# Kernel tuning notes

Measured on AMD Instinct MI355X. Metric: run time of the kernel, lower is better.

## Reference

```python
import jax, jax.numpy as jnp
import numpy as np

N, G, E, H, Z = 50000, 2000, 800000, 512, 64
BN_EPS = 1e-5


def setup_inputs() -> dict:
    key = jax.random.key(0)
    ks = jax.random.split(key, 10)
    x = jax.random.normal(ks[0], (N, G), dtype=jnp.float32)
    edge_index = jax.random.randint(ks[1], (2, E), 0, N, dtype=jnp.int32)
    s1 = 1.0 / np.sqrt(G)
    s2 = 1.0 / np.sqrt(H)
    return {
        "x": x,
        "edge_index": edge_index,
        "W1l": jax.random.normal(ks[2], (G, H), dtype=jnp.float32) * s1,
        "b1": jnp.zeros((H,), jnp.float32),
        "W1r": jax.random.normal(ks[3], (G, H), dtype=jnp.float32) * s1,
        "bn_gamma": jax.random.uniform(ks[4], (H,), dtype=jnp.float32) + 0.5,
        "bn_beta": jax.random.normal(ks[5], (H,), dtype=jnp.float32) * 0.1,
        "bn_mean": jax.random.normal(ks[6], (H,), dtype=jnp.float32) * 0.1,
        "bn_var": jax.random.uniform(ks[7], (H,), dtype=jnp.float32) + 0.5,
        "W2l": jax.random.normal(ks[8], (H, Z), dtype=jnp.float32) * s2,
        "b2": jnp.zeros((Z,), jnp.float32),
        "W2r": jax.random.normal(ks[9], (H, Z), dtype=jnp.float32) * s2,
    }


def _sage_conv(h, src, dst, Wl, bl, Wr, n_nodes):
    # mean aggregation of source features at destination nodes
    msg = h[src]  # [E, D] gather
    agg = jax.ops.segment_sum(msg, dst, num_segments=n_nodes)
    cnt = jax.ops.segment_sum(jnp.ones((src.shape[0],), h.dtype), dst, num_segments=n_nodes)
    agg = agg / jnp.maximum(cnt, 1.0)[:, None]
    # PyG SAGEConv: lin_l(agg) + lin_r(x), bias only on lin_l
    return agg @ Wl + bl + h @ Wr


def reference(x, edge_index, W1l, b1, W1r, bn_gamma, bn_beta, bn_mean, bn_var, W2l, b2, W2r):
    src, dst = edge_index[0], edge_index[1]
    n = x.shape[0]
    h = _sage_conv(x, src, dst, W1l, b1, W1r, n)  # [N, H]
    # BatchNorm1d (eval mode: running stats) + ReLU; dropout is identity at inference
    h = (h - bn_mean) * (bn_gamma / jnp.sqrt(bn_var + BN_EPS)) + bn_beta
    h = jax.nn.relu(h)
    z = _sage_conv(h, src, dst, W2l, b2, W2r, n)  # [N, Z]
    return z
```

## Files before the change

kernel.cpp:

```cpp
#include <hip/hip_runtime.h>


#define BN_EPS 1e-5f
#define GK 2000
#define KP 2048
#define NT1C 63
#define NT1P 64
#define NT2 16

typedef __attribute__((ext_vector_type(8))) short bf16x8;
typedef __attribute__((ext_vector_type(4))) float f32x4;
typedef unsigned short u16x8 __attribute__((ext_vector_type(8)));

__device__ inline unsigned short f2bf(float f) {
    union { float f; unsigned u; } v; v.f = f;
    unsigned r = (v.u + 0x7fffu + ((v.u >> 16) & 1u)) >> 16;
    return (unsigned short)r;
}
__device__ inline float bf2f(unsigned short u) {
    union { unsigned u; float f; } v; v.u = ((unsigned)u) << 16;
    return v.f;
}

#define GLL16(gp, lp) __builtin_amdgcn_global_load_lds( \
    (const __attribute__((address_space(1))) void*)(gp), \
    (__attribute__((address_space(3))) void*)(lp), 16, 0, 0)

__global__ void count_kernel(const int* __restrict__ ei, int E, int* __restrict__ cnt) {
    int i = blockIdx.x * blockDim.x + threadIdx.x;
    if (i < E) atomicAdd(&cnt[ei[E + i]], 1);
}

__global__ __launch_bounds__(1024) void scan_kernel(const int* __restrict__ cnt,
                                                    int* __restrict__ row_start, int n) {
    __shared__ int part[1024];
    int t = threadIdx.x;
    int chunk = (n + 1023) >> 10;
    int lo = t * chunk;
    int hi = lo + chunk; if (hi > n) hi = n;
    int s = 0;
    for (int i = lo; i < hi; ++i) s += cnt[i];
    part[t] = s;
    __syncthreads();
    for (int off = 1; off < 1024; off <<= 1) {
        int add = (t >= off) ? part[t - off] : 0;
        __syncthreads();
        part[t] += add;
        __syncthreads();
    }
    int run = (t == 0) ? 0 : part[t - 1];
    for (int i = lo; i < hi; ++i) { row_start[i] = run; run += cnt[i]; }
    if (t == 1023) row_start[n] = part[1023];
}

__global__ void fill_kernel(const int* __restrict__ ei, int E,
                            const int* __restrict__ row_start,
                            int* __restrict__ cnt, int* __restrict__ colidx) {
    int i = blockIdx.x * blockDim.x + threadIdx.x;
    if (i < E) {
        int d = ei[E + i];
        int p = atomicSub(&cnt[d], 1) - 1;
        colidx[row_start[d] + p] = ei[i];
    }
}

__global__ __launch_bounds__(256) void conv_kernel(const float* __restrict__ x,
                                                   unsigned short* __restrict__ xb) {
    int row = blockIdx.x;
    int k8 = threadIdx.x;
    unsigned short us[8];
    if (k8 < 250) {
        const float4* p = (const float4*)(x + (size_t)row * 2000 + k8 * 8);
        float4 v0 = p[0], v1 = p[1];
        us[0]=f2bf(v0.x); us[1]=f2bf(v0.y); us[2]=f2bf(v0.z); us[3]=f2bf(v0.w);
        us[4]=f2bf(v1.x); us[5]=f2bf(v1.y); us[6]=f2bf(v1.z); us[7]=f2bf(v1.w);
    } else {
#pragma unroll
        for (int j = 0; j < 8; ++j) us[j] = 0;
    }
    *(u16x8*)&xb[(size_t)row * 2048 + k8 * 8] = *(u16x8*)us;
}

__global__ __launch_bounds__(256) void prep_bt(const float* __restrict__ W1l,
                                               const float* __restrict__ W1r,
                                               unsigned short* __restrict__ BT) {
    int idx = blockIdx.x * 256 + threadIdx.x;
    int c  = idx >> 8;
    int k0 = (idx & 255) << 3;
    const float* W = (c < 512) ? (W1l + c) : (W1r + (c - 512));
    unsigned short us[8];
#pragma unroll
    for (int j = 0; j < 8; ++j) {
        int k = k0 + j;
        float v = (k < GK) ? W[(size_t)k * 512] : 0.0f;
        us[j] = f2bf(v);
    }
    *(u16x8*)&BT[(size_t)c * KP + k0] = *(u16x8*)us;
}

__global__ __launch_bounds__(256) void prep_bt2(const float* __restrict__ W2l,
                                                const float* __restrict__ W2r,
                                                unsigned short* __restrict__ BT2) {
    int idx = blockIdx.x * 256 + threadIdx.x;
    int c  = idx >> 6;
    int k0 = (idx & 63) << 3;
    const float* W = (c < 64) ? (W2l + c) : (W2r + (c - 64));
    unsigned short us[8];
#pragma unroll
    for (int j = 0; j < 8; ++j) us[j] = f2bf(W[(size_t)(k0 + j) * 64]);
    *(u16x8*)&BT2[(size_t)c * 512 + k0] = *(u16x8*)us;
}

__global__ __launch_bounds__(512) void gemm1_256(
    const unsigned short* __restrict__ xb, int M,
    const unsigned short* __restrict__ BT,
    unsigned short* __restrict__ Y)
{
    __shared__ __align__(16) unsigned short As[3][8192];
    __shared__ __align__(16) unsigned short Bs[3][8192];

    const int t = threadIdx.x, wid = t >> 6, lane = t & 63;
    const int nbr = (M + 255) >> 8;
    const int nwg = nbr * 4;
    const int b   = blockIdx.x;
    int swz;
    if ((nwg & 7) == 0) swz = (b & 7) * (nwg >> 3) + (b >> 3);
    else swz = b;
    const int row0 = (swz >> 2) << 8;
    const int col0 = (swz & 3) << 8;

    const int c0 = t, c1 = t + 512;
    const int g0 = ((c0 & 3) ^ ((c0 >> 3) & 3)) << 3;
    const int g1 = ((c1 & 3) ^ ((c1 >> 3) & 3)) << 3;
    int ra0 = row0 + (c0 >> 2); if (ra0 >= M) ra0 = M - 1;
    int ra1 = row0 + (c1 >> 2); if (ra1 >= M) ra1 = M - 1;
    const unsigned short* aS0 = xb + (size_t)ra0 * KP + g0;
    const unsigned short* aS1 = xb + (size_t)ra1 * KP + g1;
    const unsigned short* bS0 = BT + (size_t)(col0 + (c0 >> 2)) * KP + g0;
    const unsigned short* bS1 = BT + (size_t)(col0 + (c1 >> 2)) * KP + g1;

    const int wr = wid >> 2, wc = wid & 3;
    const int fr16 = lane & 15;
    const int gswr = ((lane >> 4) ^ ((fr16 >> 1) & 3)) << 4;

    f32x4 acc[8][4];
#pragma unroll
    for (int m = 0; m < 8; ++m)
#pragma unroll
        for (int n = 0; n < 4; ++n) acc[m][n] = (f32x4)0.0f;

#define STG(kt, buf) do {                                          \
        unsigned short* ab_ = &As[buf][0];                         \
        unsigned short* bb_ = &Bs[buf][0];                         \
        GLL16(aS0 + (size_t)(kt) * 32, ab_ + c0 * 8);              \
        GLL16(aS1 + (size_t)(kt) * 32, ab_ + c1 * 8);              \
        GLL16(bS0 + (size_t)(kt) * 32, bb_ + c0 * 8);              \
        GLL16(bS1 + (size_t)(kt) * 32, bb_ + c1 * 8);              \
    } while (0)

    STG(0, 0);
    STG(1, 1);

    int rb = 0;
    for (int it = 0; it < NT1P; ++it) {
        if (it == NT1P - 1) {
            asm volatile("s_waitcnt vmcnt(0)" ::: "memory");
        } else {
            asm volatile("s_waitcnt vmcnt(4)" ::: "memory");
        }
        __builtin_amdgcn_s_barrier();
        __builtin_amdgcn_sched_barrier(0);

        const char* Ab = (const char*)&As[rb][0];
        const char* Bb = (const char*)&Bs[rb][0];
        bf16x8 af[8], bfr[4];
#pragma unroll
        for (int m = 0; m < 8; ++m)
            af[m] = *(const bf16x8*)(Ab + ((wr * 128 + m * 16 + fr16) << 6) + gswr);
#pragma unroll
        for (int n = 0; n < 4; ++n)
            bfr[n] = *(const bf16x8*)(Bb + ((wc * 64 + n * 16 + fr16) << 6) + gswr);

        if (it + 2 < NT1P) {
            int wb = rb + 2; if (wb >= 3) wb -= 3;
            STG(it + 2, wb);
        }

        __builtin_amdgcn_s_setprio(1);
#pragma unroll
        for (int m = 0; m < 8; ++m)
#pragma unroll
            for (int n = 0; n < 4; ++n)
                acc[m][n] = __builtin_amdgcn_mfma_f32_16x16x32_bf16(
                    af[m], bfr[n], acc[m][n], 0, 0, 0);
        __builtin_amdgcn_s_setprio(0);

        rb = (rb == 2) ? 0 : rb + 1;
    }
#undef STG

    const int crow = (lane >> 4) << 2;
#pragma unroll
    for (int m = 0; m < 8; ++m) {
        int rbase = row0 + wr * 128 + m * 16 + crow;
#pragma unroll
        for (int r = 0; r < 4; ++r) {
            int row = rbase + r;
            if (row < M) {
                unsigned short* Yp = Y + (size_t)row * 1024 + col0 + wc * 64 + fr16;
#pragma unroll
                for (int n = 0; n < 4; ++n)
                    Yp[n * 16] = f2bf(acc[m][n][r]);
            }
        }
    }
}

__global__ __launch_bounds__(256) void gemm1_cvt(
    const float* __restrict__ A, int M,
    const unsigned short* __restrict__ BT,
    unsigned short* __restrict__ Y)
{
    __shared__ __align__(16) unsigned short As[128][32];
    __shared__ __align__(16) unsigned short Bs[2][128][32];

    const int t    = threadIdx.x;
    const int wid  = t >> 6;
    const int lane = t & 63;
    const int nby = (M + 127) >> 7;
    const int b   = blockIdx.x;
    const int swz = (b & 7) * nby + (b >> 3);
    const int row0 = (swz >> 3) << 7;
    const int col0 = (swz & 7) << 7;

    const int ar  = t >> 1;
    const int akq = (t & 1) << 4;
    int garow = row0 + ar; if (garow >= M) garow = M - 1;
    const float* aptr = A + (size_t)garow * GK + akq;

    const int i0 = wid * 64 + lane;
    const unsigned short* bptr0 = BT + ((size_t)(col0 + (i0 >> 2)) * KP + ((i0 & 3) << 3));
    const unsigned short* bptr1 = bptr0 + (size_t)64 * KP;

    const int wr   = wid >> 1, wc = wid & 1;
    const int fr16 = lane & 15;
    const int kb8  = (lane >> 4) << 3;

    f32x4 acc[4][4];
#pragma unroll
    for (int m = 0; m < 4; ++m)
#pragma unroll
        for (int n = 0; n < 4; ++n) acc[m][n] = (f32x4)0.0f;

    GLL16(bptr0, &Bs[0][wid * 16][0]);
    GLL16(bptr1, &Bs[0][64 + wid * 16][0]);

    float frg[16];
    {
        const float4* p = (const float4*)aptr;
        float4 v0 = p[0], v1 = p[1], v2 = p[2], v3 = p[3];
        frg[0]=v0.x; frg[1]=v0.y; frg[2]=v0.z;  frg[3]=v0.w;
        frg[4]=v1.x; frg[5]=v1.y; frg[6]=v1.z;  frg[7]=v1.w;
        frg[8]=v2.x; frg[9]=v2.y; frg[10]=v2.z; frg[11]=v2.w;
        frg[12]=v3.x;frg[13]=v3.y;frg[14]=v3.z; frg[15]=v3.w;
    }

    int cur = 0;
    for (int it = 0; it < NT1C; ++it) {
        {
            unsigned short us[16];
#pragma unroll
            for (int j = 0; j < 16; ++j) us[j] = f2bf(frg[j]);
            *(u16x8*)&As[ar][akq]     = *(u16x8*)&us[0];
            *(u16x8*)&As[ar][akq + 8] = *(u16x8*)&us[8];
        }
        __syncthreads();

        if (it + 1 < NT1C) {
            int kb = (it + 1) * 32 + akq;
            if (kb < GK) {
                const float4* p = (const float4*)(aptr + (size_t)(it + 1) * 32);
                float4 v0 = p[0], v1 = p[1], v2 = p[2], v3 = p[3];
                frg[0]=v0.x; frg[1]=v0.y; frg[2]=v0.z;  frg[3]=v0.w;
                frg[4]=v1.x; frg[5]=v1.y; frg[6]=v1.z;  frg[7]=v1.w;
                frg[8]=v2.x; frg[9]=v2.y; frg[10]=v2.z; frg[11]=v2.w;
                frg[12]=v3.x;frg[13]=v3.y;frg[14]=v3.z; frg[15]=v3.w;
            } else {
#pragma unroll
                for (int j = 0; j < 16; ++j) frg[j] = 0.0f;
            }
            const unsigned short* bp = bptr0 + (size_t)(it + 1) * 32;
            GLL16(bp,                   &Bs[cur ^ 1][wid * 16][0]);
            GLL16(bp + (size_t)64 * KP, &Bs[cur ^ 1][64 + wid * 16][0]);
        }

        bf16x8 af[4], bfr[4];
#pragma unroll
        for (int m = 0; m < 4; ++m)
            af[m] = *(const bf16x8*)&As[wr * 64 + m * 16 + fr16][kb8];
#pragma unroll
        for (int n = 0; n < 4; ++n)
            bfr[n] = *(const bf16x8*)&Bs[cur][wc * 64 + n * 16 + fr16][kb8];
#pragma unroll
        for (int m = 0; m < 4; ++m)
#pragma unroll
            for (int n = 0; n < 4; ++n)
                acc[m][n] = __builtin_amdgcn_mfma_f32_16x16x32_bf16(
                    af[m], bfr[n], acc[m][n], 0, 0, 0);

        __syncthreads();
        cur ^= 1;
    }

    const int crow = (lane >> 4) << 2;
#pragma unroll
    for (int m = 0; m < 4; ++m) {
        int rbase = row0 + wr * 64 + m * 16 + crow;
#pragma unroll
        for (int r = 0; r < 4; ++r) {
            int row = rbase + r;
            if (row < M) {
                unsigned short* Yp = Y + (size_t)row * 1024 + col0 + wc * 64 + fr16;
#pragma unroll
                for (int n = 0; n < 4; ++n)
                    Yp[n * 16] = f2bf(acc[m][n][r]);
            }
        }
    }
}

__global__ __launch_bounds__(256) void agg1_kernel(
    const unsigned short* __restrict__ Y, unsigned short* __restrict__ Hh,
    const int* __restrict__ row_start, const int* __restrict__ colidx,
    const float* __restrict__ b1, const float* __restrict__ gamma,
    const float* __restrict__ beta, const float* __restrict__ mean,
    const float* __restrict__ var, int n)
{
    int wid  = (blockIdx.x * blockDim.x + threadIdx.x) >> 6;
    int lane = threadIdx.x & 63;
    if (wid >= n) return;
    int c0 = lane * 8;
    float sc[8], sh[8], bb[8];
#pragma unroll
    for (int j = 0; j < 8; ++j) {
        int c = c0 + j;
        sc[j] = gamma[c] * rsqrtf(var[c] + BN_EPS);
        sh[j] = beta[c] - mean[c] * sc[j];
        bb[j] = b1[c];
    }
    int s0 = row_start[wid], s1 = row_start[wid + 1];
    float acc[8] = {0, 0, 0, 0, 0, 0, 0, 0};
    for (int i = s0; i < s1; ++i) {
        int src = colidx[i];
        u16x8 v = *(const u16x8*)&Y[(size_t)src * 1024 + c0];
#pragma unroll
        for (int j = 0; j < 8; ++j) acc[j] += bf2f(v[j]);
    }
    float inv = 1.0f / fmaxf((float)(s1 - s0), 1.0f);
    u16x8 sv = *(const u16x8*)&Y[(size_t)wid * 1024 + 512 + c0];
    unsigned short o[8];
#pragma unroll
    for (int j = 0; j < 8; ++j) {
        float pre = acc[j] * inv + bb[j] + bf2f(sv[j]);
        float h = pre * sc[j] + sh[j];
        o[j] = f2bf(fmaxf(h, 0.0f));
    }
    *(u16x8*)&Hh[(size_t)wid * 512 + c0] = *(u16x8*)o;
}

__global__ __launch_bounds__(256) void gemm2_bf16(
    const unsigned short* __restrict__ Hh, int M,
    const unsigned short* __restrict__ BT2,
    unsigned short* __restrict__ U)
{
    __shared__ __align__(16) unsigned short As[2][128][32];
    __shared__ __align__(16) unsigned short Bs[2][128][32];

    const int t    = threadIdx.x;
    const int wid  = t >> 6;
    const int lane = t & 63;
    const int row0 = blockIdx.x << 7;

    const int c_lo = wid * 64 + lane;
    const int c_hi = c_lo + 256;
    const int s_lo = ((c_lo & 3) ^ ((c_lo >> 3) & 3)) << 3;
    const int s_hi = ((c_hi & 3) ^ ((c_hi >> 3) & 3)) << 3;
    int ra = row0 + (c_lo >> 2); if (ra >= M) ra = M - 1;
    int rbw = row0 + (c_hi >> 2); if (rbw >= M) rbw = M - 1;
    const unsigned short* aSrc0 = Hh + (size_t)ra * 512 + s_lo;
    const unsigned short* aSrc1 = Hh + (size_t)rbw * 512 + s_hi;
    const unsigned short* bSrc0 = BT2 + (size_t)(c_lo >> 2) * 512 + s_lo;
    const unsigned short* bSrc1 = BT2 + (size_t)(c_hi >> 2) * 512 + s_hi;

    const int wr   = wid >> 1, wc = wid & 1;
    const int fr16 = lane & 15;
    const int gsw2 = ((lane >> 4) ^ ((fr16 >> 1) & 3)) << 4;

    f32x4 acc[4][4];
#pragma unroll
    for (int m = 0; m < 4; ++m)
#pragma unroll
        for (int n = 0; n < 4; ++n) acc[m][n] = (f32x4)0.0f;

#define STAGE2(kt, buf) do {                                                  \
        int ko = (kt) * 32;                                                   \
        GLL16(aSrc0 + ko, (unsigned short*)&As[buf][0][0] + (size_t)c_lo * 8);  \
        GLL16(aSrc1 + ko, (unsigned short*)&As[buf][0][0] + (size_t)c_hi * 8);  \
        GLL16(bSrc0 + ko, (unsigned short*)&Bs[buf][0][0] + (size_t)c_lo * 8);  \
        GLL16(bSrc1 + ko, (unsigned short*)&Bs[buf][0][0] + (size_t)c_hi * 8);  \
    } while (0)

    STAGE2(0, 0);
    int cur = 0;
    for (int it = 0; it < NT2; ++it) {
        __syncthreads();
        if (it + 1 < NT2) STAGE2(it + 1, cur ^ 1);

        const char* Ab = (const char*)&As[cur][0][0];
        const char* Bb = (const char*)&Bs[cur][0][0];
        bf16x8 af[4], bfr[4];
#pragma unroll
        for (int m = 0; m < 4; ++m)
            af[m] = *(const bf16x8*)(Ab + ((wr * 64 + m * 16 + fr16) << 6) + gsw2);
#pragma unroll
        for (int n = 0; n < 4; ++n)
            bfr[n] = *(const bf16x8*)(Bb + ((wc * 64 + n * 16 + fr16) << 6) + gsw2);
#pragma unroll
        for (int m = 0; m < 4; ++m)
#pragma unroll
            for (int n = 0; n < 4; ++n)
                acc[m][n] = __builtin_amdgcn_mfma_f32_16x16x32_bf16(
                    af[m], bfr[n], acc[m][n], 0, 0, 0);
        cur ^= 1;
    }
#undef STAGE2

    const int crow = (lane >> 4) << 2;
#pragma unroll
    for (int m = 0; m < 4; ++m) {
        int rbase = row0 + wr * 64 + m * 16 + crow;
#pragma unroll
        for (int r = 0; r < 4; ++r) {
            int row = rbase + r;
            if (row < M) {
                unsigned short* Up = U + (size_t)row * 128 + wc * 64 + fr16;
#pragma unroll
                for (int n = 0; n < 4; ++n)
                    Up[n * 16] = f2bf(acc[m][n][r]);
            }
        }
    }
}

__global__ __launch_bounds__(256) void agg2_kernel(
    const unsigned short* __restrict__ U,
    const int* __restrict__ row_start, const int* __restrict__ colidx,
    const float* __restrict__ b2, float* __restrict__ out, int n)
{
    int wid  = (blockIdx.x * blockDim.x + threadIdx.x) >> 6;
    int lane = threadIdx.x & 63;
    if (wid >= n) return;
    int s0 = row_start[wid], s1 = row_start[wid + 1];
    float acc = 0.f;
    for (int i = s0; i < s1; ++i) {
        int src = colidx[i];
        acc += bf2f(U[(size_t)src * 128 + lane]);
    }
    float inv = 1.0f / fmaxf((float)(s1 - s0), 1.0f);
    float z = acc * inv + b2[lane] + bf2f(U[(size_t)wid * 128 + 64 + lane]);
    out[(size_t)wid * 64 + lane] = z;
}

extern "C" void kernel_launch(void* const* d_in, const int* in_sizes, int n_in,
                              void* d_out, int out_size, void* d_ws, size_t ws_size,
                              hipStream_t stream) {
    const float* x     = (const float*)d_in[0];
    const int*   ei    = (const int*)d_in[1];
    const float* W1l   = (const float*)d_in[2];
    const float* b1    = (const float*)d_in[3];
    const float* W1r   = (const float*)d_in[4];
    const float* gamma = (const float*)d_in[5];
    const float* beta  = (const float*)d_in[6];
    const float* mean  = (const float*)d_in[7];
    const float* var   = (const float*)d_in[8];
    const float* W2l   = (const float*)d_in[9];
    const float* b2    = (const float*)d_in[10];
    const float* W2r   = (const float*)d_in[11];
    float* out = (float*)d_out;

    const int N = in_sizes[0] / 2000;
    const int E = in_sizes[1] / 2;
    const int nby = (N + 127) / 128;

    char* ws = (char*)d_ws;

    size_t need = (size_t)N * KP * 2 + (size_t)N * 1024 * 2
                + (size_t)1024 * KP * 2 + (size_t)128 * 512 * 2
                + ((size_t)2 * N + 8 + (size_t)E) * 4;

    if (ws_size >= need) {
        unsigned short* xb  = (unsigned short*)ws;
        unsigned short* Y   = xb + (size_t)N * KP;
        unsigned short* BT  = Y + (size_t)N * 1024;
        unsigned short* BT2 = BT + (size_t)1024 * KP;
        int* cnt       = (int*)(BT2 + (size_t)128 * 512);
        int* row_start = cnt + N;
        int* colidx    = row_start + N + 4;
        unsigned short* Hh = xb;
        unsigned short* U  = Y;

        hipMemsetAsync(cnt, 0, (size_t)N * sizeof(int), stream);

        prep_bt<<<1024, 256, 0, stream>>>(W1l, W1r, BT);
        prep_bt2<<<32, 256, 0, stream>>>(W2l, W2r, BT2);
        conv_kernel<<<N, 256, 0, stream>>>(x, xb);

        int eb = (E + 255) / 256;
        count_kernel<<<eb, 256, 0, stream>>>(ei, E, cnt);
        scan_kernel<<<1, 1024, 0, stream>>>(cnt, row_start, N);
        fill_kernel<<<eb, 256, 0, stream>>>(ei, E, row_start, cnt, colidx);

        int nbr = (N + 255) / 256;
        gemm1_256<<<nbr * 4, 512, 0, stream>>>(xb, N, BT, Y);
        agg1_kernel<<<(N + 3) / 4, 256, 0, stream>>>(
            Y, Hh, row_start, colidx, b1, gamma, beta, mean, var, N);
        gemm2_bf16<<<nby, 256, 0, stream>>>(Hh, N, BT2, U);
        agg2_kernel<<<(N + 3) / 4, 256, 0, stream>>>(
            U, row_start, colidx, b2, out, N);
    } else {
        unsigned short* Y   = (unsigned short*)ws;
        unsigned short* Hh  = Y + (size_t)N * 1024;
        unsigned short* U   = Hh + (size_t)N * 512;
        unsigned short* BT  = U + (size_t)N * 128;
        unsigned short* BT2 = BT + (size_t)1024 * KP;
        int* cnt       = (int*)(BT2 + (size_t)128 * 512);
        int* row_start = cnt + N;
        int* colidx    = row_start + N + 4;

        hipMemsetAsync(cnt, 0, (size_t)N * sizeof(int), stream);

        prep_bt<<<1024, 256, 0, stream>>>(W1l, W1r, BT);
        prep_bt2<<<32, 256, 0, stream>>>(W2l, W2r, BT2);

        int eb = (E + 255) / 256;
        count_kernel<<<eb, 256, 0, stream>>>(ei, E, cnt);
        scan_kernel<<<1, 1024, 0, stream>>>(cnt, row_start, N);
        fill_kernel<<<eb, 256, 0, stream>>>(ei, E, row_start, cnt, colidx);

        gemm1_cvt<<<8 * nby, 256, 0, stream>>>(x, N, BT, Y);
        agg1_kernel<<<(N + 3) / 4, 256, 0, stream>>>(
            Y, Hh, row_start, colidx, b1, gamma, beta, mean, var, N);
        gemm2_bf16<<<nby, 256, 0, stream>>>(Hh, N, BT2, U);
        agg2_kernel<<<(N + 3) / 4, 256, 0, stream>>>(
            U, row_start, colidx, b2, out, N);
    }
}
```

Before: 765.4 us.

## Split GEMM1 k-step into two half-phases interleaving A/B staging with MFMA

The main GEMM loop now loads half of the A fragments, issues the A-tile prefetch, runs the first half of the MFMAs, then hits an extra barrier, loads the second half of A, issues the B-tile prefetch and runs the remaining MFMAs. The goal is to spread global-to-LDS traffic across the iteration and lower the number of fragment registers held at once. In exchange it adds a second barrier per k-step. Separately, the fp32-to-bf16 conversion kernel becomes a grid-stride loop over 2048 blocks instead of one block per row.

```diff
diff --git a/kernel.cpp b/kernel.cpp
--- a/kernel.cpp
+++ b/kernel.cpp
@@ -65,20 +65,24 @@
 }
 
 __global__ __launch_bounds__(256) void conv_kernel(const float* __restrict__ x,
-                                                   unsigned short* __restrict__ xb) {
-    int row = blockIdx.x;
-    int k8 = threadIdx.x;
-    unsigned short us[8];
-    if (k8 < 250) {
-        const float4* p = (const float4*)(x + (size_t)row * 2000 + k8 * 8);
-        float4 v0 = p[0], v1 = p[1];
-        us[0]=f2bf(v0.x); us[1]=f2bf(v0.y); us[2]=f2bf(v0.z); us[3]=f2bf(v0.w);
-        us[4]=f2bf(v1.x); us[5]=f2bf(v1.y); us[6]=f2bf(v1.z); us[7]=f2bf(v1.w);
-    } else {
-#pragma unroll
-        for (int j = 0; j < 8; ++j) us[j] = 0;
-    }
-    *(u16x8*)&xb[(size_t)row * 2048 + k8 * 8] = *(u16x8*)us;
+                                                   unsigned short* __restrict__ xb,
+                                                   int total8) {
+    for (int idx = blockIdx.x * 256 + threadIdx.x; idx < total8;
+         idx += gridDim.x * 256) {
+        int row = idx >> 8;
+        int k8  = idx & 255;
+        unsigned short us[8];
+        if (k8 < 250) {
+            const float4* p = (const float4*)(x + (size_t)row * 2000 + k8 * 8);
+            float4 v0 = p[0], v1 = p[1];
+            us[0]=f2bf(v0.x); us[1]=f2bf(v0.y); us[2]=f2bf(v0.z); us[3]=f2bf(v0.w);
+            us[4]=f2bf(v1.x); us[5]=f2bf(v1.y); us[6]=f2bf(v1.z); us[7]=f2bf(v1.w);
+        } else {
+#pragma unroll
+            for (int j = 0; j < 8; ++j) us[j] = 0;
+        }
+        *(u16x8*)&xb[(size_t)row * 2048 + k8 * 8] = *(u16x8*)us;
+    }
 }
 
 __global__ __launch_bounds__(256) void prep_bt(const float* __restrict__ W1l,
@@ -149,17 +153,19 @@
 #pragma unroll
         for (int n = 0; n < 4; ++n) acc[m][n] = (f32x4)0.0f;
 
-#define STG(kt, buf) do {                                          \
+#define STG_A(kt, buf) do {                                        \
         unsigned short* ab_ = &As[buf][0];                         \
-        unsigned short* bb_ = &Bs[buf][0];                         \
         GLL16(aS0 + (size_t)(kt) * 32, ab_ + c0 * 8);              \
         GLL16(aS1 + (size_t)(kt) * 32, ab_ + c1 * 8);              \
+    } while (0)
+#define STG_B(kt, buf) do {                                        \
+        unsigned short* bb_ = &Bs[buf][0];                         \
         GLL16(bS0 + (size_t)(kt) * 32, bb_ + c0 * 8);              \
         GLL16(bS1 + (size_t)(kt) * 32, bb_ + c1 * 8);              \
     } while (0)
 
-    STG(0, 0);
-    STG(1, 1);
+    STG_A(0, 0); STG_B(0, 0);
+    STG_A(1, 1); STG_B(1, 1);
 
     int rb = 0;
     for (int it = 0; it < NT1P; ++it) {
@@ -173,31 +179,51 @@
 
         const char* Ab = (const char*)&As[rb][0];
         const char* Bb = (const char*)&Bs[rb][0];
-        bf16x8 af[8], bfr[4];
-#pragma unroll
-        for (int m = 0; m < 8; ++m)
-            af[m] = *(const bf16x8*)(Ab + ((wr * 128 + m * 16 + fr16) << 6) + gswr);
+        const int wb = (rb + 2 >= 3) ? rb - 1 : rb + 2;
+        const bool do_stage = (it + 2 < NT1P);
+
+        bf16x8 af0[4], bfr[4];
+#pragma unroll
+        for (int m = 0; m < 4; ++m)
+            af0[m] = *(const bf16x8*)(Ab + ((wr * 128 + m * 16 + fr16) << 6) + gswr);
 #pragma unroll
         for (int n = 0; n < 4; ++n)
             bfr[n] = *(const bf16x8*)(Bb + ((wc * 64 + n * 16 + fr16) << 6) + gswr);
 
-        if (it + 2 < NT1P) {
-            int wb = rb + 2; if (wb >= 3) wb -= 3;
-            STG(it + 2, wb);
-        }
+        if (do_stage) STG_A(it + 2, wb);
 
         __builtin_amdgcn_s_setprio(1);
 #pragma unroll
-        for (int m = 0; m < 8; ++m)
+        for (int m = 0; m < 4; ++m)
 #pragma unroll
             for (int n = 0; n < 4; ++n)
                 acc[m][n] = __builtin_amdgcn_mfma_f32_16x16x32_bf16(
-                    af[m], bfr[n], acc[m][n], 0, 0, 0);
+                    af0[m], bfr[n], acc[m][n], 0, 0, 0);
         __builtin_amdgcn_s_setprio(0);
 
+        __builtin_amdgcn_s_barrier();
+        __builtin_amdgcn_sched_barrier(0);
+
+        bf16x8 af1[4];
+#pragma unroll
+        for (int m = 0; m < 4; ++m)
+            af1[m] = *(const bf16x8*)(Ab + ((wr * 128 + (m + 4) * 16 + fr16) << 6) + gswr);
+
+        if (do_stage) STG_B(it + 2, wb);
+
+        __builtin_amdgcn_s_setprio(1);
+#pragma unroll
+        for (int m = 0; m < 4; ++m)
+#pragma unroll
+            for (int n = 0; n < 4; ++n)
+                acc[m + 4][n] = __builtin_amdgcn_mfma_f32_16x16x32_bf16(
+                    af1[m], bfr[n], acc[m + 4][n], 0, 0, 0);
+        __builtin_amdgcn_s_setprio(0);
+
         rb = (rb == 2) ? 0 : rb + 1;
     }
-#undef STG
+#undef STG_A
+#undef STG_B
 
     const int crow = (lane >> 4) << 2;
 #pragma unroll
@@ -513,7 +539,7 @@
 
         prep_bt<<<1024, 256, 0, stream>>>(W1l, W1r, BT);
         prep_bt2<<<32, 256, 0, stream>>>(W2l, W2r, BT2);
-        conv_kernel<<<N, 256, 0, stream>>>(x, xb);
+        conv_kernel<<<2048, 256, 0, stream>>>(x, xb, N * 256);
 
         int eb = (E + 255) / 256;
         count_kernel<<<eb, 256, 0, stream>>>(ei, E, cnt);
```

Result: slower. 781.9 us (+2.2%).

## Fuse prep kernels with edge counting, fold BatchNorm into W1, unroll aggregation

Applied to the files above, without the earlier changes.

The x-to-bf16 conversion, both weight transposes, the edge-degree count and a folded-bias computation are merged into one multi-role launch, so independent prep work can run concurrently. The BatchNorm scale is folded into the W1l/W1r columns and a precomputed bias b1p, which removes per-thread BN arithmetic from agg1. Both aggregation loops are unrolled by two so two neighbour gathers are in flight at once. The cost is one more bf16 rounding of the scaled weights and a more complex block-role dispatch with fixed grid-stride constants.

```diff
diff --git a/kernel.cpp b/kernel.cpp
--- a/kernel.cpp
+++ b/kernel.cpp
@@ -26,9 +26,69 @@
     (const __attribute__((address_space(1))) void*)(gp), \
     (__attribute__((address_space(3))) void*)(lp), 16, 0, 0)
 
-__global__ void count_kernel(const int* __restrict__ ei, int E, int* __restrict__ cnt) {
-    int i = blockIdx.x * blockDim.x + threadIdx.x;
-    if (i < E) atomicAdd(&cnt[ei[E + i]], 1);
+__global__ __launch_bounds__(256) void prep_fused(
+    const float* __restrict__ x, unsigned short* __restrict__ xb,
+    const float* __restrict__ W1l, const float* __restrict__ W1r,
+    const float* __restrict__ gamma, const float* __restrict__ beta,
+    const float* __restrict__ mean, const float* __restrict__ var,
+    const float* __restrict__ b1, unsigned short* __restrict__ BT,
+    const float* __restrict__ W2l, const float* __restrict__ W2r,
+    unsigned short* __restrict__ BT2, float* __restrict__ b1p,
+    const int* __restrict__ ei, int* __restrict__ cnt, int N, int E)
+{
+    const int bb = blockIdx.x;
+    if (bb < 2048) {
+        const int total8 = N * 256;
+        for (int idx = bb * 256 + threadIdx.x; idx < total8; idx += 2048 * 256) {
+            int row = idx >> 8;
+            int k8  = idx & 255;
+            unsigned short us[8];
+            if (k8 < 250) {
+                const float4* p = (const float4*)(x + (size_t)row * 2000 + k8 * 8);
+                float4 v0 = p[0], v1 = p[1];
+                us[0]=f2bf(v0.x); us[1]=f2bf(v0.y); us[2]=f2bf(v0.z); us[3]=f2bf(v0.w);
+                us[4]=f2bf(v1.x); us[5]=f2bf(v1.y); us[6]=f2bf(v1.z); us[7]=f2bf(v1.w);
+            } else {
+#pragma unroll
+                for (int j = 0; j < 8; ++j) us[j] = 0;
+            }
+            *(u16x8*)&xb[(size_t)row * 2048 + k8 * 8] = *(u16x8*)us;
+        }
+    } else if (bb < 3072) {
+        int idx = (bb - 2048) * 256 + threadIdx.x;
+        int c  = idx >> 8;
+        int k0 = (idx & 255) << 3;
+        int cc = (c < 512) ? c : c - 512;
+        float scv = gamma[cc] * rsqrtf(var[cc] + BN_EPS);
+        const float* W = (c < 512) ? (W1l + cc) : (W1r + cc);
+        unsigned short us[8];
+#pragma unroll
+        for (int j = 0; j < 8; ++j) {
+            int k = k0 + j;
+            float v = (k < GK) ? W[(size_t)k * 512] * scv : 0.0f;
+            us[j] = f2bf(v);
+        }
+        *(u16x8*)&BT[(size_t)c * KP + k0] = *(u16x8*)us;
+    } else if (bb < 3104) {
+        int idx = (bb - 3072) * 256 + threadIdx.x;
+        int c  = idx >> 6;
+        int k0 = (idx & 63) << 3;
+        const float* W = (c < 64) ? (W2l + c) : (W2r + (c - 64));
+        unsigned short us[8];
+#pragma unroll
+        for (int j = 0; j < 8; ++j) us[j] = f2bf(W[(size_t)(k0 + j) * 64]);
+        *(u16x8*)&BT2[(size_t)c * 512 + k0] = *(u16x8*)us;
+    } else if (bb == 3104) {
+#pragma unroll
+        for (int h = 0; h < 2; ++h) {
+            int c = threadIdx.x + h * 256;
+            float scv = gamma[c] * rsqrtf(var[c] + BN_EPS);
+            b1p[c] = b1[c] * scv + (beta[c] - mean[c] * scv);
+        }
+    } else {
+        for (int i = (bb - 3105) * 256 + threadIdx.x; i < E; i += 991 * 256)
+            atomicAdd(&cnt[ei[E + i]], 1);
+    }
 }
 
 __global__ __launch_bounds__(1024) void scan_kernel(const int* __restrict__ cnt,
@@ -64,53 +124,6 @@
     }
 }
 
-__global__ __launch_bounds__(256) void conv_kernel(const float* __restrict__ x,
-                                                   unsigned short* __restrict__ xb) {
-    int row = blockIdx.x;
-    int k8 = threadIdx.x;
-    unsigned short us[8];
-    if (k8 < 250) {
-        const float4* p = (const float4*)(x + (size_t)row * 2000 + k8 * 8);
-        float4 v0 = p[0], v1 = p[1];
-        us[0]=f2bf(v0.x); us[1]=f2bf(v0.y); us[2]=f2bf(v0.z); us[3]=f2bf(v0.w);
-        us[4]=f2bf(v1.x); us[5]=f2bf(v1.y); us[6]=f2bf(v1.z); us[7]=f2bf(v1.w);
-    } else {
-#pragma unroll
-        for (int j = 0; j < 8; ++j) us[j] = 0;
-    }
-    *(u16x8*)&xb[(size_t)row * 2048 + k8 * 8] = *(u16x8*)us;
-}
-
-__global__ __launch_bounds__(256) void prep_bt(const float* __restrict__ W1l,
-                                               const float* __restrict__ W1r,
-                                               unsigned short* __restrict__ BT) {
-    int idx = blockIdx.x * 256 + threadIdx.x;
-    int c  = idx >> 8;
-    int k0 = (idx & 255) << 3;
-    const float* W = (c < 512) ? (W1l + c) : (W1r + (c - 512));
-    unsigned short us[8];
-#pragma unroll
-    for (int j = 0; j < 8; ++j) {
-        int k = k0 + j;
-        float v = (k < GK) ? W[(size_t)k * 512] : 0.0f;
-        us[j] = f2bf(v);
-    }
-    *(u16x8*)&BT[(size_t)c * KP + k0] = *(u16x8*)us;
-}
-
-__global__ __launch_bounds__(256) void prep_bt2(const float* __restrict__ W2l,
-                                                const float* __restrict__ W2r,
-                                                unsigned short* __restrict__ BT2) {
-    int idx = blockIdx.x * 256 + threadIdx.x;
-    int c  = idx >> 6;
-    int k0 = (idx & 63) << 3;
-    const float* W = (c < 64) ? (W2l + c) : (W2r + (c - 64));
-    unsigned short us[8];
-#pragma unroll
-    for (int j = 0; j < 8; ++j) us[j] = f2bf(W[(size_t)(k0 + j) * 64]);
-    *(u16x8*)&BT2[(size_t)c * 512 + k0] = *(u16x8*)us;
-}
-
 __global__ __launch_bounds__(512) void gemm1_256(
     const unsigned short* __restrict__ xb, int M,
     const unsigned short* __restrict__ BT,
@@ -332,25 +345,27 @@
 __global__ __launch_bounds__(256) void agg1_kernel(
     const unsigned short* __restrict__ Y, unsigned short* __restrict__ Hh,
     const int* __restrict__ row_start, const int* __restrict__ colidx,
-    const float* __restrict__ b1, const float* __restrict__ gamma,
-    const float* __restrict__ beta, const float* __restrict__ mean,
-    const float* __restrict__ var, int n)
+    const float* __restrict__ b1p, int n)
 {
     int wid  = (blockIdx.x * blockDim.x + threadIdx.x) >> 6;
     int lane = threadIdx.x & 63;
     if (wid >= n) return;
     int c0 = lane * 8;
-    float sc[8], sh[8], bb[8];
-#pragma unroll
-    for (int j = 0; j < 8; ++j) {
-        int c = c0 + j;
-        sc[j] = gamma[c] * rsqrtf(var[c] + BN_EPS);
-        sh[j] = beta[c] - mean[c] * sc[j];
-        bb[j] = b1[c];
-    }
+    float bb[8];
+    *(float4*)&bb[0] = *(const float4*)&b1p[c0];
+    *(float4*)&bb[4] = *(const float4*)&b1p[c0 + 4];
+
     int s0 = row_start[wid], s1 = row_start[wid + 1];
     float acc[8] = {0, 0, 0, 0, 0, 0, 0, 0};
-    for (int i = s0; i < s1; ++i) {
+    int i = s0;
+    for (; i + 2 <= s1; i += 2) {
+        int src0 = colidx[i], src1 = colidx[i + 1];
+        u16x8 v0 = *(const u16x8*)&Y[(size_t)src0 * 1024 + c0];
+        u16x8 v1 = *(const u16x8*)&Y[(size_t)src1 * 1024 + c0];
+#pragma unroll
+        for (int j = 0; j < 8; ++j) acc[j] += bf2f(v0[j]) + bf2f(v1[j]);
+    }
+    if (i < s1) {
         int src = colidx[i];
         u16x8 v = *(const u16x8*)&Y[(size_t)src * 1024 + c0];
 #pragma unroll
@@ -362,8 +377,7 @@
 #pragma unroll
     for (int j = 0; j < 8; ++j) {
         float pre = acc[j] * inv + bb[j] + bf2f(sv[j]);
-        float h = pre * sc[j] + sh[j];
-        o[j] = f2bf(fmaxf(h, 0.0f));
+        o[j] = f2bf(fmaxf(pre, 0.0f));
     }
     *(u16x8*)&Hh[(size_t)wid * 512 + c0] = *(u16x8*)o;
 }
@@ -462,10 +476,12 @@
     if (wid >= n) return;
     int s0 = row_start[wid], s1 = row_start[wid + 1];
     float acc = 0.f;
-    for (int i = s0; i < s1; ++i) {
-        int src = colidx[i];
-        acc += bf2f(U[(size_t)src * 128 + lane]);
-    }
+    int i = s0;
+    for (; i + 2 <= s1; i += 2) {
+        int src0 = colidx[i], src1 = colidx[i + 1];
+        acc += bf2f(U[(size_t)src0 * 128 + lane]) + bf2f(U[(size_t)src1 * 128 + lane]);
+    }
+    if (i < s1) acc += bf2f(U[(size_t)colidx[i] * 128 + lane]);
     float inv = 1.0f / fmaxf((float)(s1 - s0), 1.0f);
     float z = acc * inv + b2[lane] + bf2f(U[(size_t)wid * 128 + 64 + lane]);
     out[(size_t)wid * 64 + lane] = z;
@@ -495,7 +511,7 @@
     char* ws = (char*)d_ws;
 
     size_t need = (size_t)N * KP * 2 + (size_t)N * 1024 * 2
-                + (size_t)1024 * KP * 2 + (size_t)128 * 512 * 2
+                + (size_t)1024 * KP * 2 + (size_t)128 * 512 * 2 + 2048
                 + ((size_t)2 * N + 8 + (size_t)E) * 4;
 
     if (ws_size >= need) {
@@ -503,7 +519,8 @@
         unsigned short* Y   = xb + (size_t)N * KP;
         unsigned short* BT  = Y + (size_t)N * 1024;
         unsigned short* BT2 = BT + (size_t)1024 * KP;
-        int* cnt       = (int*)(BT2 + (size_t)128 * 512);
+        float* b1p     = (float*)(BT2 + (size_t)128 * 512);
+        int* cnt       = (int*)(b1p + 512);
         int* row_start = cnt + N;
         int* colidx    = row_start + N + 4;
         unsigned short* Hh = xb;
@@ -511,19 +528,18 @@
 
         hipMemsetAsync(cnt, 0, (size_t)N * sizeof(int), stream);
 
-        prep_bt<<<1024, 256, 0, stream>>>(W1l, W1r, BT);
-        prep_bt2<<<32, 256, 0, stream>>>(W2l, W2r, BT2);
-        conv_kernel<<<N, 256, 0, stream>>>(x, xb);
-
+        prep_fused<<<4096, 256, 0, stream>>>(
+            x, xb, W1l, W1r, gamma, beta, mean, var, b1, BT,
+            W2l, W2r, BT2, b1p, ei, cnt, N, E);
+
+        scan_kernel<<<1, 1024, 0, stream>>>(cnt, row_start, N);
         int eb = (E + 255) / 256;
-        count_kernel<<<eb, 256, 0, stream>>>(ei, E, cnt);
-        scan_kernel<<<1, 1024, 0, stream>>>(cnt, row_start, N);
         fill_kernel<<<eb, 256, 0, stream>>>(ei, E, row_start, cnt, colidx);
 
         int nbr = (N + 255) / 256;
         gemm1_256<<<nbr * 4, 512, 0, stream>>>(xb, N, BT, Y);
         agg1_kernel<<<(N + 3) / 4, 256, 0, stream>>>(
-            Y, Hh, row_start, colidx, b1, gamma, beta, mean, var, N);
+            Y, Hh, row_start, colidx, b1p, N);
         gemm2_bf16<<<nby, 256, 0, stream>>>(Hh, N, BT2, U);
         agg2_kernel<<<(N + 3) / 4, 256, 0, stream>>>(
             U, row_start, colidx, b2, out, N);
@@ -533,23 +549,27 @@
         unsigned short* U   = Hh + (size_t)N * 512;
         unsigned short* BT  = U + (size_t)N * 128;
         unsigned short* BT2 = BT + (size_t)1024 * KP;
-        int* cnt       = (int*)(BT2 + (size_t)128 * 512);
+        float* b1p     = (float*)(BT2 + (size_t)128 * 512);
+        int* cnt       = (int*)(b1p + 512);
         int* row_start = cnt + N;
         int* colidx    = row_start + N + 4;
 
         hipMemsetAsync(cnt, 0, (size_t)N * sizeof(int), stream);
 
-        prep_bt<<<1024, 256, 0, stream>>>(W1l, W1r, BT);
-        prep_bt2<<<32, 256, 0, stream>>>(W2l, W2r, BT2);
-
+        prep_fused<<<2048, 256, 0, stream>>>(
+            x, (unsigned short*)Y , W1l, W1r, gamma, beta, mean, var,
+            b1, BT, W2l, W2r, BT2, b1p, ei, cnt, 0, 0);
+        prep_fused<<<4096, 256, 0, stream>>>(
+            x, (unsigned short*)Y, W1l, W1r, gamma, beta, mean, var,
+            b1, BT, W2l, W2r, BT2, b1p, ei, cnt, 0, E);
+
+        scan_kernel<<<1, 1024, 0, stream>>>(cnt, row_start, N);
         int eb = (E + 255) / 256;
-        count_kernel<<<eb, 256, 0, stream>>>(ei, E, cnt);
-        scan_kernel<<<1, 1024, 0, stream>>>(cnt, row_start, N);
         fill_kernel<<<eb, 256, 0, stream>>>(ei, E, row_start, cnt, colidx);
 
         gemm1_cvt<<<8 * nby, 256, 0, stream>>>(x, N, BT, Y);
         agg1_kernel<<<(N + 3) / 4, 256, 0, stream>>>(
-            Y, Hh, row_start, colidx, b1, gamma, beta, mean, var, N);
+            Y, Hh, row_start, colidx, b1p, N);
         gemm2_bf16<<<nby, 256, 0, stream>>>(Hh, N, BT2, U);
         agg2_kernel<<<(N + 3) / 4, 256, 0, stream>>>(
             U, row_start, colidx, b2, out, N);
```

Measured after the change: 701.2 us. 8.4% less time.
